# Optimization experiments

Measured on AMD Instinct MI355X. Metric: run time of the kernel, lower is better.

## Reference

```python
import jax, jax.numpy as jnp
import numpy as np

TOP_K = 8  # config.top_k


def setup_inputs() -> dict:
    key = jax.random.key(0)
    k1, k2 = jax.random.split(key)
    B, S, H, E = 4, 4096, 4096, 64
    x = jax.random.normal(k1, (B, S, H), dtype=jnp.float32)
    # nn.Linear(hidden_size, expert_num, bias=False) weight: [E, H]
    W = jax.random.normal(k2, (E, H), dtype=jnp.float32) / np.sqrt(H).astype(np.float32)
    return {"x": x, "W": W}


def reference(x, W):
    # gate linear: [B,S,H] @ [E,H]^T -> [B,S,E]
    logits = jnp.einsum('bsh,eh->bse', x, W)
    # top-k along experts
    topk_vals, indices = jax.lax.top_k(logits, TOP_K)  # [B,S,K]
    # scatter topk values into a -inf-filled tensor. Since the scattered src
    # values are exactly the logits at those indices, this equals masking.
    E = logits.shape[-1]
    mask = jax.nn.one_hot(indices, E, dtype=bool).any(axis=-2)  # [B,S,E]
    sparse_logits = jnp.where(mask, logits, -jnp.inf)
    sparse_probs = jax.nn.softmax(sparse_logits, axis=-1)  # [B,S,E]
    gate_logit = logits.reshape(-1, E)  # [B*S, E]
    return sparse_probs, indices, gate_logit
```

## Files before the change

kernel.cpp:

```cpp
#include <hip/hip_runtime.h>
#include <math.h>

#define H_DIM  4096
#define E_NUM  64
#define N_TOK  16384
#define TPB    64
#define KC     128
#define NCHUNK (H_DIM / KC)
#define TOPK   8

#define N_PROBS  (N_TOK * E_NUM)
#define N_IDX    (N_TOK * TOPK)
#define OFF_IDX  N_PROBS
#define OFF_GATE (N_PROBS + N_IDX)


typedef __attribute__((ext_vector_type(8))) __fp16 half8;
typedef __attribute__((ext_vector_type(2))) __fp16 half2t;
typedef __attribute__((ext_vector_type(16))) float f32x16;
typedef __attribute__((ext_vector_type(4))) unsigned int uint4v;

#define XSCALE 64.0f
#define WSCALE 256.0f
#define DESCALE (1.0 / 16384.0)

__global__ __launch_bounds__(512, 2)
void gating_kernel(const float* __restrict__ x, const float* __restrict__ W,
                   float* __restrict__ out) {
  __shared__ union __align__(16) {
    struct { float xs[2][64][KC]; float ws[2][64][KC]; } t;
    struct { float pad[16384]; double dump[4][16][64]; } r;
    float lg[TPB][E_NUM + 1];
  } u;

  const int tid  = threadIdx.x;
  const int tok0 = blockIdx.x * TPB;
  const int lane = tid & 63;
  const int wid  = tid >> 6;
  const int g    = wid >> 2;
  const int sub  = wid & 3;
  const int wm   = sub >> 1;
  const int wn   = sub & 1;
  const int l31  = lane & 31;
  const int arow = 32 * wm + l31;
  const int brow = 32 * wn + l31;
  const int khalf = 32 * (lane >> 5);

  const float* xg = x + (size_t)tok0 * H_DIM;

  auto stage = [&](const float* gbase, float* lds, int cbyte) {
#pragma unroll
    for (int i = 0; i < 4; ++i) {
      const int I   = i * 8 + wid;
      const int row = 2 * I + (lane >> 5);
      const int lin = (lane & 31) * 16;
      const char* src = (const char*)(gbase + (size_t)row * H_DIM) + cbyte
                        + (lin ^ ((row & 7) << 4));
      __builtin_amdgcn_global_load_lds(
          (const __attribute__((address_space(1))) unsigned int*)src,
          (__attribute__((address_space(3))) unsigned int*)((char*)lds + I * 1024),
          16, 0, 0);
    }
  };

  auto frag16 = [&](const float* base, int row, int q) -> float4 {
    return *(const float4*)((const char*)base + row * 512
                            + (q ^ ((row & 7) << 4)));
  };

  auto split8 = [&](float4 v0, float4 v1, float scale, half8& hi, half8& lo) {
    const float f[8] = {v0.x, v0.y, v0.z, v0.w, v1.x, v1.y, v1.z, v1.w};
    unsigned hu[4], lu[4];
#pragma unroll
    for (int i = 0; i < 4; ++i) {
      const float a = f[2 * i] * scale;
      const float b = f[2 * i + 1] * scale;
      half2t h = __builtin_amdgcn_cvt_pkrtz(a, b);
      const float r0 = a - (float)h.x;
      const float r1 = b - (float)h.y;
      half2t l = __builtin_amdgcn_cvt_pkrtz(r0, r1);
      hu[i] = __builtin_bit_cast(unsigned, h);
      lu[i] = __builtin_bit_cast(unsigned, l);
    }
    hi = __builtin_bit_cast(half8, (uint4v){hu[0], hu[1], hu[2], hu[3]});
    lo = __builtin_bit_cast(half8, (uint4v){lu[0], lu[1], lu[2], lu[3]});
  };

  stage(xg, &u.t.xs[0][0][0], 0);
  stage(W,  &u.t.ws[0][0][0], 0);
  __syncthreads();

  f32x16 aH, aL;
  double accd[16];
#pragma unroll
  for (int r = 0; r < 16; ++r) { aH[r] = 0.f; aL[r] = 0.f; accd[r] = 0.0; }

  for (int c = 0; c < NCHUNK; ++c) {
    const int b = c & 1;
    if (c + 1 < NCHUNK) {
      const int cb = (c + 1) * KC * 4;
      stage(xg, &u.t.xs[b ^ 1][0][0], cb);
      stage(W,  &u.t.ws[b ^ 1][0][0], cb);
    }
    const float* xt = &u.t.xs[b][0][0];
    const float* wt = &u.t.ws[b][0][0];

#pragma unroll
    for (int kt = 0; kt < 4; ++kt) {
      const int q = (4 * g + kt) * 64 + khalf;
      half8 ah, al, bh, bl;
      split8(frag16(xt, arow, q), frag16(xt, arow, q + 16), XSCALE, ah, al);
      split8(frag16(wt, brow, q), frag16(wt, brow, q + 16), WSCALE, bh, bl);
      aH = __builtin_amdgcn_mfma_f32_32x32x16_f16(ah, bh, aH, 0, 0, 0);
      aL = __builtin_amdgcn_mfma_f32_32x32x16_f16(al, bh, aL, 0, 0, 0);
      aH = __builtin_amdgcn_mfma_f32_32x32x16_f16(ah, bl, aH, 0, 0, 0);
      aL = __builtin_amdgcn_mfma_f32_32x32x16_f16(al, bl, aL, 0, 0, 0);
    }

    if (c & 1) {
#pragma unroll
      for (int r = 0; r < 16; ++r) {
        accd[r] += (double)aH[r] + (double)aL[r];
        aH[r] = 0.f; aL[r] = 0.f;
      }
    }

    __syncthreads();
  }
  __syncthreads();

  if (g == 1) {
#pragma unroll
    for (int r = 0; r < 16; ++r) u.r.dump[sub][r][lane] = accd[r];
  }
  __syncthreads();

  if (g == 0) {
    const int rb = 4 * (lane >> 5);
    float* gate = out + OFF_GATE;
#pragma unroll
    for (int q = 0; q < 4; ++q)
#pragma unroll
      for (int j = 0; j < 4; ++j) {
        const int reg   = 4 * q + j;
        const int row32 = j + 8 * q + rb;
        const float v   = (float)((accd[reg] + u.r.dump[sub][reg][lane]) * DESCALE);
        const int trow  = 32 * wm + row32;
        const int e     = 32 * wn + l31;
        gate[(size_t)(tok0 + trow) * E_NUM + e] = v;
        u.lg[trow][e] = v;
      }
  }
  __syncthreads();

  if (tid < TPB) {
    const int t = tid;
    float vals[TOPK];
    int   idxs[TOPK];
#pragma unroll
    for (int p = 0; p < TOPK; ++p) {
      float best = -INFINITY;
      int   bi   = 0;
      for (int e = 0; e < E_NUM; ++e) {
        const float v = u.lg[t][e];
        if (v > best) { best = v; bi = e; }
      }
      vals[p] = best;
      idxs[p] = bi;
      u.lg[t][bi] = -INFINITY;
    }
    const float m = vals[0];
    float s = 0.f, pr[TOPK];
#pragma unroll
    for (int p = 0; p < TOPK; ++p) { pr[p] = __expf(vals[p] - m); s += pr[p]; }
    const float inv = 1.0f / s;
    for (int e = 0; e < E_NUM; ++e) u.lg[t][e] = 0.f;
#pragma unroll
    for (int p = 0; p < TOPK; ++p) u.lg[t][idxs[p]] = pr[p] * inv;

    float* oidx = out + OFF_IDX + (size_t)(tok0 + t) * TOPK;
#pragma unroll
    for (int p = 0; p < TOPK; ++p) oidx[p] = (float)idxs[p];
  }
  __syncthreads();

  float* oprob = out + (size_t)tok0 * E_NUM;
#pragma unroll
  for (int p = 0; p < 8; ++p) {
    const int f = tid + 512 * p;
    oprob[f] = u.lg[f >> 6][f & 63];
  }
}

extern "C" void kernel_launch(void* const* d_in, const int* in_sizes, int n_in,
                              void* d_out, int out_size, void* d_ws, size_t ws_size,
                              hipStream_t stream) {
  const float* x = (const float*)d_in[0];
  const float* W = (const float*)d_in[1];
  float* out = (float*)d_out;
  dim3 grid(N_TOK / TPB);
  dim3 block(512);
  gating_kernel<<<grid, block, 0, stream>>>(x, W, out);
}
```

Before: 422.6 us.

## Use 4-stage LDS ring with vmcnt waits and drop split-K wave groups

Reduces the block to 256 threads (4 waves) and removes the two-group split-K with its LDS double reduction, so each wave computes the full K range for its 32x32 tile. The K chunk is halved to 64 and a 4-buffer LDS ring prefetches two chunks ahead. Explicit s_waitcnt vmcnt counts plus a raw s_barrier replace the per-iteration __syncthreads, aiming to overlap global loads with MFMA work. The trade-off is fewer waves per block to hide latency and hand-tuned vmcnt counts that must match the number of issued loads.

```diff
diff --git a/kernel.cpp b/kernel.cpp
--- a/kernel.cpp
+++ b/kernel.cpp
@@ -5,7 +5,7 @@
 #define E_NUM  64
 #define N_TOK  16384
 #define TPB    64
-#define KC     128
+#define KC     64
 #define NCHUNK (H_DIM / KC)
 #define TOPK   8
 
@@ -24,12 +24,11 @@
 #define WSCALE 256.0f
 #define DESCALE (1.0 / 16384.0)
 
-__global__ __launch_bounds__(512, 2)
+__global__ __launch_bounds__(256, 1)
 void gating_kernel(const float* __restrict__ x, const float* __restrict__ W,
                    float* __restrict__ out) {
   __shared__ union __align__(16) {
-    struct { float xs[2][64][KC]; float ws[2][64][KC]; } t;
-    struct { float pad[16384]; double dump[4][16][64]; } r;
+    struct { float xs[4][64][KC]; float ws[4][64][KC]; } t;
     float lg[TPB][E_NUM + 1];
   } u;
 
@@ -37,10 +36,8 @@
   const int tok0 = blockIdx.x * TPB;
   const int lane = tid & 63;
   const int wid  = tid >> 6;
-  const int g    = wid >> 2;
-  const int sub  = wid & 3;
-  const int wm   = sub >> 1;
-  const int wn   = sub & 1;
+  const int wm   = wid >> 1;
+  const int wn   = wid & 1;
   const int l31  = lane & 31;
   const int arow = 32 * wm + l31;
   const int brow = 32 * wn + l31;
@@ -51,11 +48,11 @@
   auto stage = [&](const float* gbase, float* lds, int cbyte) {
 #pragma unroll
     for (int i = 0; i < 4; ++i) {
-      const int I   = i * 8 + wid;
-      const int row = 2 * I + (lane >> 5);
-      const int lin = (lane & 31) * 16;
+      const int I   = wid * 4 + i;
+      const int row = 4 * I + (lane >> 4);
+      const int inrow = (lane & 15) * 16;
       const char* src = (const char*)(gbase + (size_t)row * H_DIM) + cbyte
-                        + (lin ^ ((row & 7) << 4));
+                        + (inrow ^ ((row & 7) << 4));
       __builtin_amdgcn_global_load_lds(
           (const __attribute__((address_space(1))) unsigned int*)src,
           (__attribute__((address_space(3))) unsigned int*)((char*)lds + I * 1024),
@@ -64,7 +61,7 @@
   };
 
   auto frag16 = [&](const float* base, int row, int q) -> float4 {
-    return *(const float4*)((const char*)base + row * 512
+    return *(const float4*)((const char*)base + row * 256
                             + (q ^ ((row & 7) << 4)));
   };
 
@@ -88,7 +85,8 @@
 
   stage(xg, &u.t.xs[0][0][0], 0);
   stage(W,  &u.t.ws[0][0][0], 0);
-  __syncthreads();
+  stage(xg, &u.t.xs[1][0][0], KC * 4);
+  stage(W,  &u.t.ws[1][0][0], KC * 4);
 
   f32x16 aH, aL;
   double accd[16];
@@ -96,18 +94,25 @@
   for (int r = 0; r < 16; ++r) { aH[r] = 0.f; aL[r] = 0.f; accd[r] = 0.0; }
 
   for (int c = 0; c < NCHUNK; ++c) {
-    const int b = c & 1;
-    if (c + 1 < NCHUNK) {
-      const int cb = (c + 1) * KC * 4;
-      stage(xg, &u.t.xs[b ^ 1][0][0], cb);
-      stage(W,  &u.t.ws[b ^ 1][0][0], cb);
+    if (c + 2 < NCHUNK) {
+      const int nb = (c + 2) & 3;
+      const int cb = (c + 2) * KC * 4;
+      stage(xg, &u.t.xs[nb][0][0], cb);
+      stage(W,  &u.t.ws[nb][0][0], cb);
     }
+    if (c + 2 < NCHUNK)      asm volatile("s_waitcnt vmcnt(16)" ::: "memory");
+    else if (c + 1 < NCHUNK) asm volatile("s_waitcnt vmcnt(8)"  ::: "memory");
+    else                     asm volatile("s_waitcnt vmcnt(0)"  ::: "memory");
+    __builtin_amdgcn_s_barrier();
+    asm volatile("" ::: "memory");
+
+    const int b = c & 3;
     const float* xt = &u.t.xs[b][0][0];
     const float* wt = &u.t.ws[b][0][0];
 
 #pragma unroll
     for (int kt = 0; kt < 4; ++kt) {
-      const int q = (4 * g + kt) * 64 + khalf;
+      const int q = kt * 64 + khalf;
       half8 ah, al, bh, bl;
       split8(frag16(xt, arow, q), frag16(xt, arow, q + 16), XSCALE, ah, al);
       split8(frag16(wt, brow, q), frag16(wt, brow, q + 16), WSCALE, bh, bl);
@@ -124,33 +129,23 @@
         aH[r] = 0.f; aL[r] = 0.f;
       }
     }
-
-    __syncthreads();
   }
   __syncthreads();
 
-  if (g == 1) {
+  const int rb = 4 * (lane >> 5);
+  float* gate = out + OFF_GATE;
 #pragma unroll
-    for (int r = 0; r < 16; ++r) u.r.dump[sub][r][lane] = accd[r];
-  }
-  __syncthreads();
-
-  if (g == 0) {
-    const int rb = 4 * (lane >> 5);
-    float* gate = out + OFF_GATE;
+  for (int q = 0; q < 4; ++q)
 #pragma unroll
-    for (int q = 0; q < 4; ++q)
-#pragma unroll
-      for (int j = 0; j < 4; ++j) {
-        const int reg   = 4 * q + j;
-        const int row32 = j + 8 * q + rb;
-        const float v   = (float)((accd[reg] + u.r.dump[sub][reg][lane]) * DESCALE);
-        const int trow  = 32 * wm + row32;
-        const int e     = 32 * wn + l31;
-        gate[(size_t)(tok0 + trow) * E_NUM + e] = v;
-        u.lg[trow][e] = v;
-      }
-  }
+    for (int j = 0; j < 4; ++j) {
+      const int reg   = 4 * q + j;
+      const int row32 = j + 8 * q + rb;
+      const float v   = (float)(accd[reg] * DESCALE);
+      const int trow  = 32 * wm + row32;
+      const int e     = 32 * wn + l31;
+      gate[(size_t)(tok0 + trow) * E_NUM + e] = v;
+      u.lg[trow][e] = v;
+    }
   __syncthreads();
 
   if (tid < TPB) {
@@ -186,8 +181,8 @@
 
   float* oprob = out + (size_t)tok0 * E_NUM;
 #pragma unroll
-  for (int p = 0; p < 8; ++p) {
-    const int f = tid + 512 * p;
+  for (int p = 0; p < 16; ++p) {
+    const int f = tid + 256 * p;
     oprob[f] = u.lg[f >> 6][f & 63];
   }
 }
@@ -199,6 +194,6 @@
   const float* W = (const float*)d_in[1];
   float* out = (float*)d_out;
   dim3 grid(N_TOK / TPB);
-  dim3 block(512);
+  dim3 block(256);
   gating_kernel<<<grid, block, 0, stream>>>(x, W, out);
 }
```

Result: faster. 401.7 us (-4.9%).
